# Kernel tuning notes

Hardware: AMD Instinct MI355X
Metric: run time of the kernel (lower is better)

## Reference

```python
import jax, jax.numpy as jnp
import numpy as np
import math

WP, WF = 10, 10      # past/future window
EPS = 1e-8           # torch cosine_similarity eps
CLIP = 1.0 - 1e-6    # keep arccos (and its grad) finite
MAXN = 110           # hard-coded alpha width in the module


def setup_inputs() -> dict:
    key = jax.random.key(0)
    k1, k2, k3, k4, k5, k6 = jax.random.split(key, 6)
    B, L, G, N, D = 32, 110, 512, 40, 300
    node_features = jax.random.normal(k1, (B, L, G), jnp.float32)
    knowledge = jax.random.normal(k2, (B, L, N, D), jnp.float32)
    anew = jax.random.uniform(k3, (B, L, N), jnp.float32)
    var_sem = 2.0 / (G + G)
    var_con = 2.0 / (D + D)
    weight_sem = jax.random.normal(k4, (G, G), jnp.float32) * var_sem
    weight_con = jax.random.normal(k5, (D, D), jnp.float32) * var_con
    text_len = jax.random.randint(k6, (B,), 55, L + 1, jnp.int32)
    return dict(node_features=node_features, knowledge=knowledge, anew=anew,
                weight_sem=weight_sem, weight_con=weight_con, text_len=text_len)


def reference(node_features, knowledge, anew, weight_sem, weight_con, text_len):
    B, L, G = node_features.shape
    N = knowledge.shape[2]
    dt = node_features.dtype

    # window + validity mask, replaces per-(i,j) python slicing: [B, j, k]
    j = jnp.arange(L)[:, None]
    k = jnp.arange(L)[None, :]
    cur = text_len[:, None, None]
    mask = (k >= j - WP) & (k <= j + WF)
    mask = mask[None] & (k[None, :, :] <= cur - 1) & (j[None, :, :] < cur)
    fmask = mask.astype(dt)

    # ---- semantic branch: score = 1 - acos(cos_sim(f_j, W_sem f_k))/pi, windowed softmax
    att_sem = jnp.einsum('st,blt->bls', weight_sem, node_features)      # [B,L,G]
    num = jnp.einsum('bjg,bkg->bjk', node_features, att_sem)
    nf = jnp.maximum(jnp.linalg.norm(node_features, axis=-1), EPS)      # [B,L]
    na = jnp.maximum(jnp.linalg.norm(att_sem, axis=-1), EPS)            # [B,L]
    cos = num / (nf[:, :, None] * na[:, None, :])
    score = 1.0 - jnp.arccos(jnp.clip(cos, -CLIP, CLIP)) / math.pi
    neg = jnp.finfo(dt).min
    s = jnp.where(mask, score, neg)
    s = s - jnp.max(s, axis=-1, keepdims=True)
    e = jnp.exp(s) * fmask
    alphas_sem = e / jnp.maximum(jnp.sum(e, axis=-1, keepdims=True), EPS)  # [B,L,L]

    # ---- affinity transform of anew: v -> (||[v, v/2] - [0.5, 0]|| - 0.06467)/0.607468
    anew_aff = (jnp.sqrt((anew - 0.5) ** 2 + (0.5 * anew) ** 2) - 0.06467) / 0.607468

    # ---- contextual branch: windowed sum_n |cos_sim(aff_feat_{k,n}, knowledge_{j,n})|
    att_con = jnp.einsum('blns,st->blnt', knowledge, weight_con)        # [B,L,N,D]
    aff_feat = att_con * anew_aff[..., None]                            # [B,L,N,D]
    num_c = jnp.einsum('bknd,bjnd->bjkn', aff_feat, knowledge)          # [B,j,k,N]
    n_f = jnp.maximum(jnp.linalg.norm(aff_feat, axis=-1), EPS)          # [B,k,N]
    n_k = jnp.maximum(jnp.linalg.norm(knowledge, axis=-1), EPS)         # [B,j,N]
    cos_c = num_c / (n_f[:, None, :, :] * n_k[:, :, None, :])
    alphas_con = 10.0 * jnp.sum(jnp.abs(cos_c), axis=-1) * fmask        # [B,j,k]

    out = 0.5 * alphas_sem + 0.5 * alphas_con                           # [B,L,L]
    if L < MAXN:  # module hard-codes width 110
        out = jnp.pad(out, ((0, 0), (0, 0), (0, MAXN - L)))
    return out
```

## Files before the change

kernel.cpp:

```cpp
#include <hip/hip_runtime.h>
#include <hip/hip_bf16.h>
#include <math.h>

constexpr int Bb   = 32;
constexpr int Ls   = 110;
constexpr int Gs   = 512;
constexpr int Ns   = 40;
constexpr int Ds   = 300;
constexpr int WPc  = 10;
constexpr int WFc  = 10;
constexpr int MAXNc = 110;
constexpr float EPSf  = 1e-8f;
constexpr float CLIPf = 1.0f - 1e-6f;
constexpr int BL = Bb * Ls;
constexpr int Mrows = BL * Ns;
constexpr int KST = 320;
constexpr int RGRP = Mrows / 256;

typedef __attribute__((ext_vector_type(8))) short short8_t;
typedef __attribute__((ext_vector_type(4))) short short4_t;
typedef __attribute__((ext_vector_type(4))) float floatx4;

__device__ __forceinline__ unsigned short bf16r(float f) {
  unsigned u = __float_as_uint(f);
  u += 0x7fffu + ((u >> 16) & 1u);
  return (unsigned short)(u >> 16);
}

__device__ __forceinline__ unsigned pkbf(float lo, float hi) {
  unsigned a = __float_as_uint(lo), b = __float_as_uint(hi);
  a += 0x7fffu + ((a >> 16) & 1u);
  b += 0x7fffu + ((b >> 16) & 1u);
  return (a >> 16) | (b & 0xffff0000u);
}

__device__ __forceinline__ short8_t cvt8(const float4 v0, const float4 v1) {
  union { short8_t s; unsigned u[4]; } p;
  p.u[0] = pkbf(v0.x, v0.y);
  p.u[1] = pkbf(v0.z, v0.w);
  p.u[2] = pkbf(v1.x, v1.y);
  p.u[3] = pkbf(v1.z, v1.w);
  return p.s;
}

__global__ __launch_bounds__(256) void transpose_wsem(const float* __restrict__ w,
                                                      float* __restrict__ wt) {
  __shared__ float tile[32][33];
  const int bx = blockIdx.x * 32;
  const int by = blockIdx.y * 32;
  const int tx = threadIdx.x;
  const int ty = threadIdx.y;
#pragma unroll
  for (int r = ty; r < 32; r += 8)
    tile[r][tx] = w[(by + r) * Gs + (bx + tx)];
  __syncthreads();
#pragma unroll
  for (int r = ty; r < 32; r += 8)
    wt[(bx + r) * Gs + (by + tx)] = tile[tx][r];
}

__global__ __launch_bounds__(64) void wctf_prep(const float* __restrict__ wc,
                                                short* __restrict__ wctf) {
  const int fid = blockIdx.x;
  const int nb = fid / 10, c = fid % 10;
  const int lane = threadIdx.x;
  const int t = nb * 16 + (lane & 15);
  const int s0 = c * 32 + (lane >> 4) * 8;
  short8_t v;
#pragma unroll
  for (int e = 0; e < 8; ++e) {
    const int s = s0 + e;
    const float f = (s < Ds && t < Ds) ? wc[s * Ds + t] : 0.f;
    v[e] = (short)bf16r(f);
  }
  *reinterpret_cast<short8_t*>(wctf + ((size_t)fid * 64 + lane) * 8) = v;
}

__global__ __launch_bounds__(256) void kn_prep(const float* __restrict__ kn,
                                               unsigned short* __restrict__ knb,
                                               float* __restrict__ kninv) {
  const int wid = (blockIdx.x * 256 + threadIdx.x) >> 6;
  const int lane = threadIdx.x & 63;
  const int nwaves = gridDim.x * 4;
  for (int row = wid; row < Mrows; row += nwaves) {
    const float* __restrict__ src = kn + (size_t)row * Ds;
    float4 v0 = make_float4(0.f, 0.f, 0.f, 0.f);
    float4 v1 = v0;
    const int d0 = lane * 8;
    if (lane < 37) {
      v0 = *reinterpret_cast<const float4*>(src + d0);
      v1 = *reinterpret_cast<const float4*>(src + d0 + 4);
    } else if (lane == 37) {
      v0 = *reinterpret_cast<const float4*>(src + d0);
    }
    float ss = v0.x * v0.x + v0.y * v0.y + v0.z * v0.z + v0.w * v0.w +
               v1.x * v1.x + v1.y * v1.y + v1.z * v1.z + v1.w * v1.w;
#pragma unroll
    for (int off = 32; off > 0; off >>= 1) ss += __shfl_xor(ss, off);
    if (lane < 40)
      *reinterpret_cast<short8_t*>(knb + (size_t)row * KST + d0) = cvt8(v0, v1);
    if (lane == 0) kninv[row] = 1.0f / fmaxf(sqrtf(ss), EPSf);
  }
}

__global__ __launch_bounds__(512) void sem_gemm(const float* __restrict__ nf,
                                                const float* __restrict__ wt,
                                                float* __restrict__ att_sem,
                                                float* __restrict__ na_arr) {
  const int bl0 = blockIdx.x * 8;
  const int s = threadIdx.x;
  const float* __restrict__ x0 = nf + (size_t)bl0 * Gs;
  float acc[8];
#pragma unroll
  for (int r = 0; r < 8; ++r) acc[r] = 0.f;
#pragma unroll 4
  for (int t = 0; t < Gs; ++t) {
    const float wv = wt[t * Gs + s];
#pragma unroll
    for (int r = 0; r < 8; ++r) acc[r] = fmaf(wv, x0[r * Gs + t], acc[r]);
  }
#pragma unroll
  for (int r = 0; r < 8; ++r) att_sem[(size_t)(bl0 + r) * Gs + s] = acc[r];

  __shared__ float partial[8][8];
  const int wave = s >> 6, lane = s & 63;
#pragma unroll
  for (int r = 0; r < 8; ++r) {
    float v = acc[r] * acc[r];
#pragma unroll
    for (int off = 32; off > 0; off >>= 1) v += __shfl_xor(v, off);
    if (lane == 0) partial[r][wave] = v;
  }
  __syncthreads();
  if (s < 8) {
    float sum = 0.f;
#pragma unroll
    for (int w2 = 0; w2 < 8; ++w2) sum += partial[s][w2];
    na_arr[bl0 + s] = fmaxf(sqrtf(sum), EPSf);
  }
}

__global__ __launch_bounds__(256) void sem_attn(const float* __restrict__ nf,
                                                const float* __restrict__ att_sem,
                                                const float* __restrict__ na_arr,
                                                const int* __restrict__ tlen,
                                                float* __restrict__ out) {
  const int blk = blockIdx.x;
  const int b = blk / Ls, j = blk % Ls;
  const int len = tlen[b];
  float* __restrict__ orow = out + (size_t)(b * Ls + j) * MAXNc;
  if (j >= len) {
    for (int k = threadIdx.x; k < MAXNc; k += 256) orow[k] = 0.f;
    return;
  }
  const int k0 = max(j - WPc, 0);
  const int k1 = min(j + WFc, len - 1);
  const int nk = k1 - k0 + 1;

  __shared__ float xs[Gs];
  __shared__ float sc[21];
  __shared__ float red[4];

  const float* __restrict__ x = nf + (size_t)(b * Ls + j) * Gs;
  float ss = 0.f;
  for (int t = threadIdx.x; t < Gs; t += 256) {
    const float v = x[t];
    xs[t] = v;
    ss += v * v;
  }
  const int wave = threadIdx.x >> 6, lane = threadIdx.x & 63;
#pragma unroll
  for (int off = 32; off > 0; off >>= 1) ss += __shfl_xor(ss, off);
  if (lane == 0) red[wave] = ss;
  __syncthreads();
  const float nfn = fmaxf(sqrtf(red[0] + red[1] + red[2] + red[3]), EPSf);

  for (int i = wave; i < nk; i += 4) {
    const int k = k0 + i;
    const float* __restrict__ as = att_sem + (size_t)(b * Ls + k) * Gs;
    float d = 0.f;
#pragma unroll
    for (int t = lane; t < Gs; t += 64) d = fmaf(xs[t], as[t], d);
#pragma unroll
    for (int off = 32; off > 0; off >>= 1) d += __shfl_xor(d, off);
    if (lane == 0) {
      float cs = d / (nfn * na_arr[b * Ls + k]);
      cs = fminf(fmaxf(cs, -CLIPf), CLIPf);
      sc[i] = 1.0f - acosf(cs) * (float)(1.0 / M_PI);
    }
  }
  __syncthreads();
  if (threadIdx.x == 0) {
    float m = -1e30f;
    for (int i = 0; i < nk; ++i) m = fmaxf(m, sc[i]);
    red[0] = m;
  }
  __syncthreads();
  const float m = red[0];
  if ((int)threadIdx.x < nk) sc[threadIdx.x] = expf(sc[threadIdx.x] - m);
  __syncthreads();
  if (threadIdx.x == 0) {
    float s = 0.f;
    for (int i = 0; i < nk; ++i) s += sc[i];
    red[1] = 1.0f / fmaxf(s, EPSf);
  }
  __syncthreads();
  const float inv = red[1];
  for (int k = threadIdx.x; k < MAXNc; k += 256) {
    float v = 0.f;
    if (k >= k0 && k <= k1) v = 0.5f * sc[k - k0] * inv;
    orow[k] = v;
  }
}

__global__ __launch_bounds__(256, 3) void con_gemm_mfma(const unsigned short* __restrict__ knb,
                                                        const short* __restrict__ wctf,
                                                        const int* __restrict__ tlen,
                                                        unsigned short* __restrict__ ybar,
                                                        float* __restrict__ rowss) {
  const int lin = blockIdx.x;
  const int xcd = lin & 7, slot = lin >> 3;
  const int m = slot & 3;
  const int g = xcd + 8 * (slot >> 2);
  if (g >= RGRP) return;
  const int rowbase = g * 256;
  const int n0 = m * 80;

  const int tid = threadIdx.x;
  const int wave = tid >> 6, lane = tid & 63;
  const int quad = lane >> 4, l16 = lane & 15;
  const int wrow = rowbase + wave * 64;

  {
    bool any = false;
    for (int bl = wrow / Ns; bl <= (wrow + 63) / Ns; ++bl)
      any |= (bl % Ls) < tlen[bl / Ls];
    if (!any) return;
  }

  const short* __restrict__ bbase = wctf + (size_t)(m * 5) * 5120;

  const unsigned short* arow[4];
#pragma unroll
  for (int tt = 0; tt < 4; ++tt)
    arow[tt] = knb + (size_t)(wrow + tt * 16 + l16) * KST + quad * 8;

  floatx4 acc[4][5];
#pragma unroll
  for (int tt = 0; tt < 4; ++tt)
#pragma unroll
    for (int i = 0; i < 5; ++i) acc[tt][i] = (floatx4){0.f, 0.f, 0.f, 0.f};

  short8_t A[2][4];
#pragma unroll
  for (int tt = 0; tt < 4; ++tt)
    A[0][tt] = *reinterpret_cast<const short8_t*>(arow[tt]);

#pragma unroll
  for (int c = 0; c < 10; ++c) {
    short8_t bfr[5];
#pragma unroll
    for (int i = 0; i < 5; ++i)
      bfr[i] = *reinterpret_cast<const short8_t*>(
          bbase + ((size_t)(i * 10 + c) * 64 + lane) * 8);
    if (c < 9) {
#pragma unroll
      for (int tt = 0; tt < 4; ++tt)
        A[(c + 1) & 1][tt] =
            *reinterpret_cast<const short8_t*>(arow[tt] + (c + 1) * 32);
    }
#pragma unroll
    for (int i = 0; i < 5; ++i)
#pragma unroll
      for (int tt = 0; tt < 4; ++tt)
        acc[tt][i] = __builtin_amdgcn_mfma_f32_16x16x32_bf16(A[c & 1][tt], bfr[i],
                                                             acc[tt][i], 0, 0, 0);
  }

#pragma unroll
  for (int tt = 0; tt < 4; ++tt) {
    const int row0 = wrow + tt * 16;
    const int blA = row0 / Ns, blB = (row0 + 15) / Ns;
    const bool alive = ((blA % Ls) < tlen[blA / Ls]) | ((blB % Ls) < tlen[blB / Ls]);
    if (!alive) continue;

#pragma unroll
    for (int r = 0; r < 4; ++r) {
      float p = 0.f;
#pragma unroll
      for (int i = 0; i < 5; ++i) p = fmaf(acc[tt][i][r], acc[tt][i][r], p);
      p += __shfl_xor(p, 1);
      p += __shfl_xor(p, 2);
      p += __shfl_xor(p, 4);
      p += __shfl_xor(p, 8);
      if (l16 == 0) atomicAdd(&rowss[row0 + quad * 4 + r], p);
    }
#pragma unroll
    for (int i = 0; i < 5; ++i) {
      const int col = n0 + i * 16 + l16;
#pragma unroll
      for (int r = 0; r < 4; ++r)
        ybar[(size_t)(row0 + quad * 4 + r) * KST + col] = bf16r(acc[tt][i][r]);
    }
  }
}

__global__ __launch_bounds__(512) void con_attn_mfma(const unsigned short* __restrict__ knb,
                                                     const unsigned short* __restrict__ ybar,
                                                     const float* __restrict__ rowss,
                                                     const float* __restrict__ kninv,
                                                     const float* __restrict__ anew,
                                                     const int* __restrict__ tlen,
                                                     float* __restrict__ out) {
  const int lin = blockIdx.x;
  const int xcd = lin & 7, slot = lin >> 3;
  const int b = xcd * 4 + slot / 7;
  const int jt = slot % 7;
  const int j0 = jt * 16;
  const int len = tlen[b];
  if (j0 >= len) return;
  const int kbase = min(max(j0 - WPc, 0), Ls - 48);

  const int tid = threadIdx.x;
  const int wave = tid >> 6, lane = tid & 63;
  const int quad = lane >> 4, l16 = lane & 15;

  __shared__ float red[8][768];

  const int jj = min(j0 + l16, Ls - 1);
  const size_t blj = (size_t)(b * Ls + jj);

  float outacc[3][4];
#pragma unroll
  for (int t = 0; t < 3; ++t)
#pragma unroll
    for (int r = 0; r < 4; ++r) outacc[t][r] = 0.f;

  const unsigned short* yrow[3];
  int krow_m[3];
#pragma unroll
  for (int t = 0; t < 3; ++t) {
    const int k = kbase + t * 16 + l16;
    yrow[t] = ybar + (size_t)(b * Ls + k) * Ns * KST;
    krow_m[t] = (b * Ls + k) * Ns;
  }

  for (int ni = 0; ni < 5; ++ni) {
    const int n = wave + ni * 8;
    const unsigned short* __restrict__ arow =
        knb + ((blj * Ns + n) * (size_t)KST) + quad * 8;

    float w_t[3];
#pragma unroll
    for (int t = 0; t < 3; ++t) {
      const int mm = krow_m[t] + n;
      const float a = anew[mm];
      const float ssqk = rowss[mm];
      const float aff = (sqrtf((a - 0.5f) * (a - 0.5f) + 0.25f * a * a) - 0.06467f) *
                        (1.0f / 0.607468f);
      w_t[t] = aff / fmaxf(aff * sqrtf(ssqk), EPSf);
    }
    const float kinv = kninv[blj * Ns + n];

    floatx4 S[3];
#pragma unroll
    for (int t = 0; t < 3; ++t) S[t] = (floatx4){0.f, 0.f, 0.f, 0.f};

#pragma unroll
    for (int c = 0; c < 10; ++c) {
      const short8_t afrag = *reinterpret_cast<const short8_t*>(arow + c * 32);
#pragma unroll
      for (int t = 0; t < 3; ++t) {
        const short8_t bfrag = *reinterpret_cast<const short8_t*>(
            yrow[t] + (size_t)n * KST + c * 32 + quad * 8);
        S[t] = __builtin_amdgcn_mfma_f32_16x16x32_bf16(afrag, bfrag, S[t], 0, 0, 0);
      }
    }

#pragma unroll
    for (int r = 0; r < 4; ++r) {
      const float kv = __shfl(kinv, quad * 4 + r);
#pragma unroll
      for (int t = 0; t < 3; ++t)
        outacc[t][r] = fmaf(kv * w_t[t], fabsf(S[t][r]), outacc[t][r]);
    }
  }

#pragma unroll
  for (int t = 0; t < 3; ++t)
#pragma unroll
    for (int r = 0; r < 4; ++r)
      red[wave][(quad * 4 + r) * 48 + t * 16 + l16] = outacc[t][r];
  __syncthreads();

  for (int idx = tid; idx < 768; idx += 512) {
    float s = 0.f;
#pragma unroll
    for (int w = 0; w < 8; ++w) s += red[w][idx];
    const int j = j0 + idx / 48;
    const int k = kbase + idx % 48;
    if (j < len && k < len && k >= j - WPc && k <= j + WFc)
      out[(size_t)(b * Ls + j) * MAXNc + k] += 5.0f * s;
  }
}

extern "C" void kernel_launch(void* const* d_in, const int* in_sizes, int n_in,
                              void* d_out, int out_size, void* d_ws, size_t ws_size,
                              hipStream_t stream) {
  const float* nf   = (const float*)d_in[0];
  const float* kn   = (const float*)d_in[1];
  const float* anew = (const float*)d_in[2];
  const float* wsem = (const float*)d_in[3];
  const float* wcon = (const float*)d_in[4];
  const int*   tlen = (const int*)d_in[5];
  float* out = (float*)d_out;

  float* att_sem = (float*)d_ws;
  float* na_arr  = att_sem + (size_t)BL * Gs;
  float* wt      = na_arr + BL;
  short* wctf    = (short*)(wt + (size_t)Gs * Gs);
  float* rowss   = (float*)(wctf + 200 * 64 * 8);
  float* kninv   = rowss + Mrows;
  unsigned short* knb  = (unsigned short*)(kninv + Mrows);
  unsigned short* ybar = knb + (size_t)Mrows * KST;

  hipMemsetAsync(rowss, 0, (size_t)Mrows * sizeof(float), stream);
  transpose_wsem<<<dim3(16, 16), dim3(32, 8), 0, stream>>>(wsem, wt);
  wctf_prep<<<200, 64, 0, stream>>>(wcon, wctf);
  kn_prep<<<2048, 256, 0, stream>>>(kn, knb, kninv);
  sem_gemm<<<BL / 8, 512, 0, stream>>>(nf, wt, att_sem, na_arr);
  sem_attn<<<BL, 256, 0, stream>>>(nf, att_sem, na_arr, tlen, out);
  con_gemm_mfma<<<2208, 256, 0, stream>>>(knb, wctf, tlen, ybar, rowss);
  con_attn_mfma<<<Bb * 7, 512, 0, stream>>>(knb, ybar, rowss, kninv, anew, tlen, out);
}
```

Before: 502.8 us.

## Fuse knowledge bf16 conversion and norm computation into contextual GEMM kernel

Removes the separate kn_prep pass. The contextual MFMA GEMM now reads fp32 knowledge directly, converts it to bf16 in registers, and accumulates per-row sums of squares. The m==0 column-group blocks write the bf16 copy and the inverse norms that the attention kernel needs. This avoids one full read of the large knowledge tensor plus a write-and-reread of its bf16 copy. In exchange, each of the four column groups fetches fp32 data (twice the bytes per load) and register pressure goes up, so launch bounds drop from 3 to 2 blocks per CU. Rows belonging to fully dead waves no longer get knb or kninv written.

```diff
diff --git a/kernel.cpp b/kernel.cpp
--- a/kernel.cpp
+++ b/kernel.cpp
@@ -18,7 +18,6 @@
 constexpr int RGRP = Mrows / 256;
 
 typedef __attribute__((ext_vector_type(8))) short short8_t;
-typedef __attribute__((ext_vector_type(4))) short short4_t;
 typedef __attribute__((ext_vector_type(4))) float floatx4;
 
 __device__ __forceinline__ unsigned short bf16r(float f) {
@@ -74,33 +73,6 @@
     v[e] = (short)bf16r(f);
   }
   *reinterpret_cast<short8_t*>(wctf + ((size_t)fid * 64 + lane) * 8) = v;
-}
-
-__global__ __launch_bounds__(256) void kn_prep(const float* __restrict__ kn,
-                                               unsigned short* __restrict__ knb,
-                                               float* __restrict__ kninv) {
-  const int wid = (blockIdx.x * 256 + threadIdx.x) >> 6;
-  const int lane = threadIdx.x & 63;
-  const int nwaves = gridDim.x * 4;
-  for (int row = wid; row < Mrows; row += nwaves) {
-    const float* __restrict__ src = kn + (size_t)row * Ds;
-    float4 v0 = make_float4(0.f, 0.f, 0.f, 0.f);
-    float4 v1 = v0;
-    const int d0 = lane * 8;
-    if (lane < 37) {
-      v0 = *reinterpret_cast<const float4*>(src + d0);
-      v1 = *reinterpret_cast<const float4*>(src + d0 + 4);
-    } else if (lane == 37) {
-      v0 = *reinterpret_cast<const float4*>(src + d0);
-    }
-    float ss = v0.x * v0.x + v0.y * v0.y + v0.z * v0.z + v0.w * v0.w +
-               v1.x * v1.x + v1.y * v1.y + v1.z * v1.z + v1.w * v1.w;
-#pragma unroll
-    for (int off = 32; off > 0; off >>= 1) ss += __shfl_xor(ss, off);
-    if (lane < 40)
-      *reinterpret_cast<short8_t*>(knb + (size_t)row * KST + d0) = cvt8(v0, v1);
-    if (lane == 0) kninv[row] = 1.0f / fmaxf(sqrtf(ss), EPSf);
-  }
 }
 
 __global__ __launch_bounds__(512) void sem_gemm(const float* __restrict__ nf,
@@ -213,11 +185,13 @@
   }
 }
 
-__global__ __launch_bounds__(256, 3) void con_gemm_mfma(const unsigned short* __restrict__ knb,
-                                                        const short* __restrict__ wctf,
-                                                        const int* __restrict__ tlen,
-                                                        unsigned short* __restrict__ ybar,
-                                                        float* __restrict__ rowss) {
+__global__ __launch_bounds__(256, 2) void con_stage(const float* __restrict__ kn,
+                                                    const short* __restrict__ wctf,
+                                                    const int* __restrict__ tlen,
+                                                    unsigned short* __restrict__ knb,
+                                                    float* __restrict__ kninv,
+                                                    unsigned short* __restrict__ ybar,
+                                                    float* __restrict__ rowss) {
   const int lin = blockIdx.x;
   const int xcd = lin & 7, slot = lin >> 3;
   const int m = slot & 3;
@@ -240,21 +214,33 @@
 
   const short* __restrict__ bbase = wctf + (size_t)(m * 5) * 5120;
 
-  const unsigned short* arow[4];
+  const float* arow[4];
+  unsigned short* krow[4];
+#pragma unroll
+  for (int tt = 0; tt < 4; ++tt) {
+    const int row = wrow + tt * 16 + l16;
+    arow[tt] = kn + (size_t)row * Ds + quad * 8;
+    krow[tt] = knb + (size_t)row * KST + quad * 8;
+  }
+
+  floatx4 acc[4][5];
 #pragma unroll
   for (int tt = 0; tt < 4; ++tt)
-    arow[tt] = knb + (size_t)(wrow + tt * 16 + l16) * KST + quad * 8;
-
-  floatx4 acc[4][5];
-#pragma unroll
-  for (int tt = 0; tt < 4; ++tt)
 #pragma unroll
     for (int i = 0; i < 5; ++i) acc[tt][i] = (floatx4){0.f, 0.f, 0.f, 0.f};
 
-  short8_t A[2][4];
-#pragma unroll
-  for (int tt = 0; tt < 4; ++tt)
-    A[0][tt] = *reinterpret_cast<const short8_t*>(arow[tt]);
+  float ssq[4] = {0.f, 0.f, 0.f, 0.f};
+
+  short8_t Af[2][4];
+#pragma unroll
+  for (int tt = 0; tt < 4; ++tt) {
+    const float4 v0 = *reinterpret_cast<const float4*>(arow[tt]);
+    const float4 v1 = *reinterpret_cast<const float4*>(arow[tt] + 4);
+    ssq[tt] += v0.x * v0.x + v0.y * v0.y + v0.z * v0.z + v0.w * v0.w +
+               v1.x * v1.x + v1.y * v1.y + v1.z * v1.z + v1.w * v1.w;
+    Af[0][tt] = cvt8(v0, v1);
+    if (m == 0) *reinterpret_cast<short8_t*>(krow[tt]) = Af[0][tt];
+  }
 
 #pragma unroll
   for (int c = 0; c < 10; ++c) {
@@ -263,23 +249,59 @@
     for (int i = 0; i < 5; ++i)
       bfr[i] = *reinterpret_cast<const short8_t*>(
           bbase + ((size_t)(i * 10 + c) * 64 + lane) * 8);
+    float4 F0[4], F1[4];
+    if (c < 8) {
+#pragma unroll
+      for (int tt = 0; tt < 4; ++tt) {
+        F0[tt] = *reinterpret_cast<const float4*>(arow[tt] + (c + 1) * 32);
+        F1[tt] = *reinterpret_cast<const float4*>(arow[tt] + (c + 1) * 32 + 4);
+      }
+    } else if (c == 8) {
+#pragma unroll
+      for (int tt = 0; tt < 4; ++tt) {
+        float4 v0 = make_float4(0.f, 0.f, 0.f, 0.f);
+        float4 v1 = make_float4(0.f, 0.f, 0.f, 0.f);
+        if (quad == 0) {
+          v0 = *reinterpret_cast<const float4*>(arow[tt] + 288);
+          v1 = *reinterpret_cast<const float4*>(arow[tt] + 292);
+        } else if (quad == 1) {
+          v0 = *reinterpret_cast<const float4*>(arow[tt] + 288);
+        }
+        F0[tt] = v0;
+        F1[tt] = v1;
+      }
+    }
+#pragma unroll
+    for (int i = 0; i < 5; ++i)
+#pragma unroll
+      for (int tt = 0; tt < 4; ++tt)
+        acc[tt][i] = __builtin_amdgcn_mfma_f32_16x16x32_bf16(Af[c & 1][tt], bfr[i],
+                                                             acc[tt][i], 0, 0, 0);
     if (c < 9) {
 #pragma unroll
-      for (int tt = 0; tt < 4; ++tt)
-        A[(c + 1) & 1][tt] =
-            *reinterpret_cast<const short8_t*>(arow[tt] + (c + 1) * 32);
-    }
-#pragma unroll
-    for (int i = 0; i < 5; ++i)
-#pragma unroll
-      for (int tt = 0; tt < 4; ++tt)
-        acc[tt][i] = __builtin_amdgcn_mfma_f32_16x16x32_bf16(A[c & 1][tt], bfr[i],
-                                                             acc[tt][i], 0, 0, 0);
+      for (int tt = 0; tt < 4; ++tt) {
+        ssq[tt] += F0[tt].x * F0[tt].x + F0[tt].y * F0[tt].y +
+                   F0[tt].z * F0[tt].z + F0[tt].w * F0[tt].w +
+                   F1[tt].x * F1[tt].x + F1[tt].y * F1[tt].y +
+                   F1[tt].z * F1[tt].z + F1[tt].w * F1[tt].w;
+        Af[(c + 1) & 1][tt] = cvt8(F0[tt], F1[tt]);
+        if (m == 0)
+          *reinterpret_cast<short8_t*>(krow[tt] + (c + 1) * 32) =
+              Af[(c + 1) & 1][tt];
+      }
+    }
   }
 
 #pragma unroll
   for (int tt = 0; tt < 4; ++tt) {
     const int row0 = wrow + tt * 16;
+
+    float sq = ssq[tt];
+    sq += __shfl_xor(sq, 16);
+    sq += __shfl_xor(sq, 32);
+    if (m == 0 && lane < 16)
+      kninv[row0 + lane] = 1.0f / fmaxf(sqrtf(sq), EPSf);
+
     const int blA = row0 / Ns, blB = (row0 + 15) / Ns;
     const bool alive = ((blA % Ls) < tlen[blA / Ls]) | ((blB % Ls) < tlen[blB / Ls]);
     if (!alive) continue;
@@ -427,9 +449,8 @@
   hipMemsetAsync(rowss, 0, (size_t)Mrows * sizeof(float), stream);
   transpose_wsem<<<dim3(16, 16), dim3(32, 8), 0, stream>>>(wsem, wt);
   wctf_prep<<<200, 64, 0, stream>>>(wcon, wctf);
-  kn_prep<<<2048, 256, 0, stream>>>(kn, knb, kninv);
   sem_gemm<<<BL / 8, 512, 0, stream>>>(nf, wt, att_sem, na_arr);
   sem_attn<<<BL, 256, 0, stream>>>(nf, att_sem, na_arr, tlen, out);
-  con_gemm_mfma<<<2208, 256, 0, stream>>>(knb, wctf, tlen, ybar, rowss);
+  con_stage<<<2208, 256, 0, stream>>>(kn, wctf, tlen, knb, kninv, ybar, rowss);
   con_attn_mfma<<<Bb * 7, 512, 0, stream>>>(knb, ybar, rowss, kninv, anew, tlen, out);
 }
```

New measurement: 699.0 us. +39.0%, slower.
